# Kernel tuning notes

Hardware: AMD Instinct MI355X
Metric: run time of the kernel (lower is better)

The kernel has to match this reference:

```python
import jax, jax.numpy as jnp
import numpy as np

BETA = 0.1
MARGIN = 0.1
LOSS_WEIGHT = 1.0
K = 4          # num_negative_samples_per_positive
EPS = 1e-6
C, D, P = 100000, 256, 65536


def _energy(p, c):
    """Euclidean entailment-cone energy: relu(apex_angle(p,c) - aperture(p))."""
    diff = c - p
    num = jnp.sum(c * c, -1) - jnp.sum(p * p, -1) - jnp.sum(diff * diff, -1)
    norm_p = jnp.linalg.norm(p, axis=-1)
    denom = 2.0 * norm_p * jnp.linalg.norm(diff, axis=-1) + EPS
    cosang = jnp.clip(num / denom, -1.0 + EPS, 1.0 - EPS)
    ang = jnp.arccos(cosang)
    aperture = jnp.arcsin(jnp.clip(BETA / (norm_p + EPS), 0.0, 1.0 - EPS))
    return jax.nn.relu(ang - aperture)


def setup_inputs() -> dict:
    key = jax.random.key(0)
    k1, k2, k3 = jax.random.split(key, 3)
    prototypes = jax.random.normal(k1, (C, D), dtype=jnp.float32)
    pairs = jax.random.randint(k2, (P, 2), 0, C, dtype=jnp.int32)
    neg_c = jax.random.randint(k3, (P * K,), 0, C, dtype=jnp.int32)
    return {"prototypes": prototypes, "pairs": pairs, "neg_c": neg_c}


def reference(prototypes, pairs, neg_c):
    # positive pairs: (parent, child) gathers
    p_pos = prototypes[pairs[:, 0]]                    # [P, D]
    c_pos = prototypes[pairs[:, 1]]                    # [P, D]
    avg_pos = _energy(p_pos, c_pos).mean()

    # negatives: each positive parent repeated K times vs sampled neg children
    neg_p_idx = jnp.repeat(pairs[:, 0], K)             # [P*K]
    p_neg = prototypes[neg_p_idx]                      # [P*K, D]
    c_neg = prototypes[neg_c]                          # [P*K, D]
    avg_neg = jax.nn.relu(MARGIN - _energy(p_neg, c_neg)).mean()

    return (avg_pos + avg_neg) * 0.5 * LOSS_WEIGHT
```

## Files before the change

### kernel.cpp

```cpp
#include <hip/hip_runtime.h>

#define BETA   0.1f
#define MARGIN 0.1f
#define EPSF   1e-6f
#define KNEG   4
#define NBINS  256

__device__ __forceinline__ float wave_sum(float v) {
    #pragma unroll
    for (int off = 32; off >= 1; off >>= 1)
        v += __shfl_xor(v, off, 64);
    return v;
}

__global__ __launch_bounds__(256) void cone_main(
    const float* __restrict__ proto,
    const int*   __restrict__ pairs,
    const int*   __restrict__ negc,
    float*       __restrict__ bins,
    int P)
{
    const int lane = threadIdx.x & 63;
    const int wid  = threadIdx.x >> 6;
    const int pair = blockIdx.x * 4 + wid;

    float pos_e = 0.f, neg_e = 0.f;
    if (pair < P) {
        const int pi = pairs[2 * pair];
        int idx[5];
        idx[0] = pairs[2 * pair + 1];
        #pragma unroll
        for (int k = 0; k < KNEG; ++k) idx[1 + k] = negc[4 * pair + k];

        float4 p = ((const float4*)(proto + (size_t)pi * 256))[lane];
        float4 cv[5];
        #pragma unroll
        for (int j = 0; j < 5; ++j)
            cv[j] = ((const float4*)(proto + (size_t)idx[j] * 256))[lane];

        float p2     = wave_sum(p.x*p.x + p.y*p.y + p.z*p.z + p.w*p.w);
        float norm_p = sqrtf(p2);
        float apert  = asinf(fminf(fmaxf(BETA / (norm_p + EPSF), 0.f), 1.f - EPSF));

        #pragma unroll
        for (int j = 0; j < 5; ++j) {
            float4 c = cv[j];
            float dx = c.x - p.x, dy = c.y - p.y, dz = c.z - p.z, dw = c.w - p.w;
            float c2 = wave_sum(c.x*c.x + c.y*c.y + c.z*c.z + c.w*c.w);
            float d2 = wave_sum(dx*dx + dy*dy + dz*dz + dw*dw);
            float num    = c2 - p2 - d2;
            float denom  = 2.f * norm_p * sqrtf(d2) + EPSF;
            float cosang = fminf(fmaxf(num / denom, -1.f + EPSF), 1.f - EPSF);
            float e      = fmaxf(acosf(cosang) - apert, 0.f);
            if (j == 0) pos_e = e;
            else        neg_e += fmaxf(MARGIN - e, 0.f);
        }
    }

    __shared__ float sp[4], sn[4];
    if (lane == 0) { sp[wid] = pos_e; sn[wid] = neg_e; }
    __syncthreads();
    if (threadIdx.x == 0) {
        float ps = sp[0] + sp[1] + sp[2] + sp[3];
        float ns = sn[0] + sn[1] + sn[2] + sn[3];
        const int b = blockIdx.x & (NBINS - 1);
        atomicAdd(&bins[b],         ps);
        atomicAdd(&bins[NBINS + b], ns);
    }
}

__global__ __launch_bounds__(256) void cone_zero(float* __restrict__ bins) {
    bins[threadIdx.x] = 0.f;
    bins[NBINS + threadIdx.x] = 0.f;
}

__global__ __launch_bounds__(256) void cone_final(
    const float* __restrict__ bins, float* __restrict__ out, int P)
{
    const int t = threadIdx.x, lane = t & 63, wid = t >> 6;
    float ps = wave_sum(bins[t]);
    float ns = wave_sum(bins[NBINS + t]);
    __shared__ float sp[4], sn[4];
    if (lane == 0) { sp[wid] = ps; sn[wid] = ns; }
    __syncthreads();
    if (t == 0) {
        float tp = sp[0] + sp[1] + sp[2] + sp[3];
        float tn = sn[0] + sn[1] + sn[2] + sn[3];
        float fP = (float)P;
        out[0] = (tp / fP + tn / (fP * (float)KNEG)) * 0.5f;
    }
}

extern "C" void kernel_launch(void* const* d_in, const int* in_sizes, int n_in,
                              void* d_out, int out_size, void* d_ws, size_t ws_size,
                              hipStream_t stream) {
    const float* proto = (const float*)d_in[0];
    const int*   pairs = (const int*)d_in[1];
    const int*   negc  = (const int*)d_in[2];
    float*       bins  = (float*)d_ws;
    const int P = in_sizes[1] / 2;

    cone_zero<<<1, NBINS, 0, stream>>>(bins);
    cone_main<<<(P + 3) / 4, 256, 0, stream>>>(proto, pairs, negc, bins, P);
    cone_final<<<1, 256, 0, stream>>>(bins, (float*)d_out, P);
}
```

Baseline: 182.7 us.

## Process four pairs per wave with 16-lane groups and deterministic partials

Each wavefront now handles four pairs, with one 16-lane group per pair, and each lane loads four float4 chunks per row. This cuts cross-lane reductions to four shuffle steps and spreads the scalar acos/asin tail math across four times as many pairs per wave. The atomic bin accumulation and its zeroing kernel are replaced by per-block partial sums written to workspace and reduced by a single 1024-thread final kernel, which removes one launch and the atomics. Each lane now holds more registers (20 float4 for children), which could lower occupancy.

Result: no change. 180.1 us (-1.5%).

```diff
diff --git a/kernel.cpp b/kernel.cpp
--- a/kernel.cpp
+++ b/kernel.cpp
@@ -4,7 +4,13 @@
 #define MARGIN 0.1f
 #define EPSF   1e-6f
 #define KNEG   4
-#define NBINS  256
+
+__device__ __forceinline__ float gsum16(float v) {
+    #pragma unroll
+    for (int off = 8; off >= 1; off >>= 1)
+        v += __shfl_xor(v, off, 64);
+    return v;
+}
 
 __device__ __forceinline__ float wave_sum(float v) {
     #pragma unroll
@@ -13,16 +19,22 @@
     return v;
 }
 
+__device__ __forceinline__ float dot4(float4 a, float4 b) {
+    return a.x*b.x + a.y*b.y + a.z*b.z + a.w*b.w;
+}
+
 __global__ __launch_bounds__(256) void cone_main(
     const float* __restrict__ proto,
     const int*   __restrict__ pairs,
     const int*   __restrict__ negc,
-    float*       __restrict__ bins,
+    float*       __restrict__ part,
     int P)
 {
     const int lane = threadIdx.x & 63;
     const int wid  = threadIdx.x >> 6;
-    const int pair = blockIdx.x * 4 + wid;
+    const int sub  = lane >> 4;
+    const int sl   = lane & 15;
+    const int pair = (blockIdx.x * 4 + wid) * 4 + sub;
 
     float pos_e = 0.f, neg_e = 0.f;
     if (pair < P) {
@@ -32,22 +44,38 @@
         #pragma unroll
         for (int k = 0; k < KNEG; ++k) idx[1 + k] = negc[4 * pair + k];
 
-        float4 p = ((const float4*)(proto + (size_t)pi * 256))[lane];
-        float4 cv[5];
+        const float4* prow = (const float4*)(proto + (size_t)pi * 256);
+        float4 pv[4];
         #pragma unroll
-        for (int j = 0; j < 5; ++j)
-            cv[j] = ((const float4*)(proto + (size_t)idx[j] * 256))[lane];
+        for (int r = 0; r < 4; ++r) pv[r] = prow[sl + 16 * r];
 
-        float p2     = wave_sum(p.x*p.x + p.y*p.y + p.z*p.z + p.w*p.w);
+        float4 cv[5][4];
+        #pragma unroll
+        for (int j = 0; j < 5; ++j) {
+            const float4* crow = (const float4*)(proto + (size_t)idx[j] * 256);
+            #pragma unroll
+            for (int r = 0; r < 4; ++r) cv[j][r] = crow[sl + 16 * r];
+        }
+
+        float pp = 0.f;
+        #pragma unroll
+        for (int r = 0; r < 4; ++r) pp += dot4(pv[r], pv[r]);
+        float p2     = gsum16(pp);
         float norm_p = sqrtf(p2);
         float apert  = asinf(fminf(fmaxf(BETA / (norm_p + EPSF), 0.f), 1.f - EPSF));
 
         #pragma unroll
         for (int j = 0; j < 5; ++j) {
-            float4 c = cv[j];
-            float dx = c.x - p.x, dy = c.y - p.y, dz = c.z - p.z, dw = c.w - p.w;
-            float c2 = wave_sum(c.x*c.x + c.y*c.y + c.z*c.z + c.w*c.w);
-            float d2 = wave_sum(dx*dx + dy*dy + dz*dz + dw*dw);
+            float cc = 0.f, dd = 0.f;
+            #pragma unroll
+            for (int r = 0; r < 4; ++r) {
+                float4 c = cv[j][r], p = pv[r];
+                cc += dot4(c, c);
+                float dx = c.x - p.x, dy = c.y - p.y, dz = c.z - p.z, dw = c.w - p.w;
+                dd += dx*dx + dy*dy + dz*dz + dw*dw;
+            }
+            float c2 = gsum16(cc);
+            float d2 = gsum16(dd);
             float num    = c2 - p2 - d2;
             float denom  = 2.f * norm_p * sqrtf(d2) + EPSF;
             float cosang = fminf(fmaxf(num / denom, -1.f + EPSF), 1.f - EPSF);
@@ -57,35 +85,36 @@
         }
     }
 
-    __shared__ float sp[4], sn[4];
-    if (lane == 0) { sp[wid] = pos_e; sn[wid] = neg_e; }
+    __shared__ float sp[16], sn[16];
+    if (sl == 0) { sp[wid * 4 + sub] = pos_e; sn[wid * 4 + sub] = neg_e; }
     __syncthreads();
     if (threadIdx.x == 0) {
-        float ps = sp[0] + sp[1] + sp[2] + sp[3];
-        float ns = sn[0] + sn[1] + sn[2] + sn[3];
-        const int b = blockIdx.x & (NBINS - 1);
-        atomicAdd(&bins[b],         ps);
-        atomicAdd(&bins[NBINS + b], ns);
+        float ps = 0.f, ns = 0.f;
+        #pragma unroll
+        for (int i = 0; i < 16; ++i) { ps += sp[i]; ns += sn[i]; }
+        part[2 * blockIdx.x]     = ps;
+        part[2 * blockIdx.x + 1] = ns;
     }
 }
 
-__global__ __launch_bounds__(256) void cone_zero(float* __restrict__ bins) {
-    bins[threadIdx.x] = 0.f;
-    bins[NBINS + threadIdx.x] = 0.f;
-}
-
-__global__ __launch_bounds__(256) void cone_final(
-    const float* __restrict__ bins, float* __restrict__ out, int P)
+__global__ __launch_bounds__(1024) void cone_final(
+    const float* __restrict__ part, float* __restrict__ out, int nblocks, int P)
 {
-    const int t = threadIdx.x, lane = t & 63, wid = t >> 6;
-    float ps = wave_sum(bins[t]);
-    float ns = wave_sum(bins[NBINS + t]);
-    __shared__ float sp[4], sn[4];
+    float ps = 0.f, ns = 0.f;
+    for (int i = threadIdx.x; i < nblocks; i += 1024) {
+        ps += part[2 * i];
+        ns += part[2 * i + 1];
+    }
+    ps = wave_sum(ps);
+    ns = wave_sum(ns);
+    const int lane = threadIdx.x & 63, wid = threadIdx.x >> 6;
+    __shared__ float sp[16], sn[16];
     if (lane == 0) { sp[wid] = ps; sn[wid] = ns; }
     __syncthreads();
-    if (t == 0) {
-        float tp = sp[0] + sp[1] + sp[2] + sp[3];
-        float tn = sn[0] + sn[1] + sn[2] + sn[3];
+    if (threadIdx.x == 0) {
+        float tp = 0.f, tn = 0.f;
+        #pragma unroll
+        for (int i = 0; i < 16; ++i) { tp += sp[i]; tn += sn[i]; }
         float fP = (float)P;
         out[0] = (tp / fP + tn / (fP * (float)KNEG)) * 0.5f;
     }
@@ -97,10 +126,10 @@
     const float* proto = (const float*)d_in[0];
     const int*   pairs = (const int*)d_in[1];
     const int*   negc  = (const int*)d_in[2];
-    float*       bins  = (float*)d_ws;
+    float*       part  = (float*)d_ws;
     const int P = in_sizes[1] / 2;
+    const int nblocks = (P + 15) / 16;
 
-    cone_zero<<<1, NBINS, 0, stream>>>(bins);
-    cone_main<<<(P + 3) / 4, 256, 0, stream>>>(proto, pairs, negc, bins, P);
-    cone_final<<<1, 256, 0, stream>>>(bins, (float*)d_out, P);
+    cone_main<<<nblocks, 256, 0, stream>>>(proto, pairs, negc, part, P);
+    cone_final<<<1, 1024, 0, stream>>>(part, (float*)d_out, nblocks, P);
 }
```
